# Kernel optimization log

Hardware: AMD Instinct MI355X
Metric: run time of the kernel (lower is better)

The kernel has to match this reference:

```python
import jax, jax.numpy as jnp
import numpy as np

N = 50000   # nodes
E = 600000  # edges
IN = 128    # in_channels
H = 128     # hidden
G = 64      # graphs in batch


def setup_inputs() -> dict:
    key = jax.random.key(0)
    ks = jax.random.split(key, 12)
    x = jax.random.normal(ks[0], (N, IN), jnp.float32)
    edge_index = jax.random.randint(ks[1], (2, E), 0, N, dtype=jnp.int64)
    batch = jnp.sort(jax.random.randint(ks[2], (N,), 0, G, dtype=jnp.int64))

    def glorot(k, i, o):
        return jax.random.normal(k, (i, o), jnp.float32) / np.float32(np.sqrt(i))

    return {
        "x": x, "edge_index": edge_index, "batch": batch,
        "W1": glorot(ks[3], IN, H), "b1": jnp.zeros((H,), jnp.float32),
        "W2": glorot(ks[4], H, H),  "b2": jnp.zeros((H,), jnp.float32),
        "W3": glorot(ks[5], H, H),  "b3": jnp.zeros((H,), jnp.float32),
        "Wl": glorot(ks[6], H, 2),  "bl": jnp.zeros((2,), jnp.float32),
    }


def gcn_conv(x, W, b, src, dst, n):
    # PyG GCNConv: linear transform, add self-loops, symmetric deg^-1/2 norm, scatter-add.
    h = x @ W                                   # [n, H]
    loop = jnp.arange(n, dtype=src.dtype)
    s = jnp.concatenate([src, loop])            # [E+n]
    d = jnp.concatenate([dst, loop])
    deg = jax.ops.segment_sum(jnp.ones_like(d, jnp.float32), d, num_segments=n)
    dinv = jax.lax.rsqrt(deg)                   # deg >= 1 thanks to self-loops
    norm = dinv[s] * dinv[d]                    # [E+n]
    out = jax.ops.segment_sum(h[s] * norm[:, None], d, num_segments=n)
    return out + b


def reference(x, edge_index, batch, W1, b1, W2, b2, W3, b3, Wl, bl):
    src, dst = edge_index[0], edge_index[1]
    h = jax.nn.relu(gcn_conv(x, W1, b1, src, dst, N))
    h = jax.nn.relu(gcn_conv(h, W2, b2, src, dst, N))
    h = jax.nn.relu(gcn_conv(h, W3, b3, src, dst, N))
    # global_mean_pool over graph ids
    cnt = jax.ops.segment_sum(jnp.ones((N,), jnp.float32), batch, num_segments=G)
    pooled = jax.ops.segment_sum(h, batch, num_segments=G) / jnp.maximum(cnt, 1.0)[:, None]
    # dropout is identity in eval mode
    return pooled @ Wl + bl                     # [G, 2]
```

## Files before the change

### kernel.cpp

```cpp
#include <hip/hip_runtime.h>


#define THREADS 256
#define ELLW 48
#define ELLS 64

typedef __attribute__((ext_vector_type(8))) short short8;
typedef __attribute__((ext_vector_type(4))) float f32x4;

__device__ inline unsigned short bf16_1(float a) {
    unsigned u = __float_as_uint(a);
    u += 0x7FFF + ((u >> 16) & 1);
    return (unsigned short)(u >> 16);
}
__device__ inline void bf16_split(float f, unsigned short& hi, unsigned short& lo) {
    unsigned u = __float_as_uint(f);
    unsigned r = u + 0x7FFF + ((u >> 16) & 1);
    hi = (unsigned short)(r >> 16);
    float hf = __uint_as_float((unsigned)hi << 16);
    float lf = f - hf;
    unsigned ul = __float_as_uint(lf);
    lo = (unsigned short)((ul + 0x7FFF + ((ul >> 16) & 1)) >> 16);
}
__device__ inline unsigned pack_bf16(float a, float b) {
    unsigned ua = __float_as_uint(a);
    unsigned ub = __float_as_uint(b);
    ua += 0x7FFF + ((ua >> 16) & 1);
    ub += 0x7FFF + ((ub >> 16) & 1);
    return (ua >> 16) | (ub & 0xFFFF0000u);
}

__global__ __launch_bounds__(THREADS) void prep_k(const float* __restrict__ W1,
                                                  const float* __restrict__ W2,
                                                  const float* __restrict__ W3,
                                                  unsigned* __restrict__ wf,
                                                  const int* __restrict__ batch,
                                                  int* __restrict__ gstart,
                                                  int* __restrict__ ell,
                                                  int n, int gtot) {
    int b = blockIdx.x;
    if (b < 3) {
        const float* W = (b == 0) ? W1 : (b == 1) ? W2 : W3;
        unsigned* o_hi = wf + (size_t)b * 16384;
        unsigned* o_lo = o_hi + 8192;
        for (int o = threadIdx.x; o < 8192; o += THREADS) {
            int d = o & 3, l = (o >> 2) & 63, ts = o >> 8;
            int s = ts & 3, t = ts >> 2;
            int k = s * 32 + ((l >> 4) << 3) + d * 2;
            int nn = t * 16 + (l & 15);
            float v0 = W[k * 128 + nn];
            float v1 = W[(k + 1) * 128 + nn];
            unsigned short h0, l0, h1, l1;
            bf16_split(v0, h0, l0);
            bf16_split(v1, h1, l1);
            o_hi[o] = (unsigned)h0 | ((unsigned)h1 << 16);
            o_lo[o] = (unsigned)l0 | ((unsigned)l1 << 16);
        }
    } else if (b == 3) {
        int t = threadIdx.x;
        if (t <= gtot) {
            int lo = 0, hi = n;
            while (lo < hi) {
                int mid = (lo + hi) >> 1;
                if (batch[mid] < t) lo = mid + 1; else hi = mid;
            }
            gstart[t] = lo;
        }
    } else {
        int i = (b - 4) * THREADS + threadIdx.x;
        if (i < n) ell[(size_t)i * ELLS] = 0;
    }
}

__global__ __launch_bounds__(THREADS) void ell_fill_k(const int* __restrict__ src,
                                                      const int* __restrict__ dst,
                                                      int* __restrict__ ell, int e) {
    int i = blockIdx.x * THREADS + threadIdx.x;
    if (i < e) {
        int d = dst[i];
        int* row = ell + (size_t)d * ELLS;
        int pos = atomicAdd(row, 1);
        if (pos < ELLW) row[1 + pos] = src[i];
    }
}

template <bool ABF16>
__global__ __launch_bounds__(THREADS) void mfma_gemm_k(const void* __restrict__ Av,
                                                       const unsigned* __restrict__ wf,
                                                       const int* __restrict__ ell,
                                                       unsigned short* __restrict__ g16u,
                                                       int n) {
    __shared__ unsigned wls[16384];
    int tid = threadIdx.x;
    int lane = tid & 63;
    int r0 = blockIdx.x * 64 + (tid >> 6) * 16;

    for (int i = tid; i < 4096; i += THREADS)
        ((uint4*)wls)[i] = ((const uint4*)wf)[i];

    f32x4 acc[8];
#pragma unroll
    for (int t = 0; t < 8; ++t) acc[t] = (f32x4){0.f, 0.f, 0.f, 0.f};

    int arow = min(r0 + (lane & 15), n - 1);
    int kcol = (lane >> 4) << 3;

    short8 ah[4], al[4];
    if (ABF16) {
        const unsigned short* A = (const unsigned short*)Av;
#pragma unroll
        for (int s = 0; s < 4; ++s)
            ah[s] = *(const short8*)&A[(size_t)arow * 128 + kcol + s * 32];
    } else {
        const float* A = (const float*)Av;
        float4 v0[4], v1[4];
#pragma unroll
        for (int s = 0; s < 4; ++s) {
            v0[s] = *(const float4*)&A[(size_t)arow * 128 + kcol + s * 32];
            v1[s] = *(const float4*)&A[(size_t)arow * 128 + kcol + s * 32 + 4];
        }
#pragma unroll
        for (int s = 0; s < 4; ++s) {
            unsigned short h[8], lo[8];
            bf16_split(v0[s].x, h[0], lo[0]); bf16_split(v0[s].y, h[1], lo[1]);
            bf16_split(v0[s].z, h[2], lo[2]); bf16_split(v0[s].w, h[3], lo[3]);
            bf16_split(v1[s].x, h[4], lo[4]); bf16_split(v1[s].y, h[5], lo[5]);
            bf16_split(v1[s].z, h[6], lo[6]); bf16_split(v1[s].w, h[7], lo[7]);
#pragma unroll
            for (int j = 0; j < 8; ++j) { ah[s][j] = (short)h[j]; al[s][j] = (short)lo[j]; }
        }
    }

    __syncthreads();

#pragma unroll
    for (int s = 0; s < 4; ++s) {
#pragma unroll
        for (int t = 0; t < 8; ++t) {
            int base = (t * 4 + s) * 256 + lane * 4;
            short8 bh = *(short8*)&wls[base];
            short8 bl = *(short8*)&wls[8192 + base];
            acc[t] = __builtin_amdgcn_mfma_f32_16x16x32_bf16(ah[s], bh, acc[t], 0, 0, 0);
            if (!ABF16)
                acc[t] = __builtin_amdgcn_mfma_f32_16x16x32_bf16(al[s], bh, acc[t], 0, 0, 0);
            acc[t] = __builtin_amdgcn_mfma_f32_16x16x32_bf16(ah[s], bl, acc[t], 0, 0, 0);
        }
    }

    int rbase = r0 + ((lane >> 4) << 2);
#pragma unroll
    for (int reg = 0; reg < 4; ++reg) {
        int rr = rbase + reg;
        if (rr < n) {
            float dv = rsqrtf(1.f + (float)ell[(size_t)rr * ELLS]);
#pragma unroll
            for (int t = 0; t < 8; ++t)
                g16u[(size_t)rr * 128 + t * 16 + (lane & 15)] = bf16_1(acc[t][reg] * dv);
        }
    }
}

__global__ __launch_bounds__(THREADS) void aggregate_k(const unsigned* __restrict__ g16,
                                                       const int* __restrict__ ell,
                                                       const float* __restrict__ bias,
                                                       unsigned* __restrict__ h16,
                                                       int n) {
    int wave = (blockIdx.x * THREADS + threadIdx.x) >> 6;
    int lane = threadIdx.x & 63;
    if (wave >= n) return;

    int v = ell[(size_t)wave * ELLS + lane];
    int cnt_true = __shfl(v, 0);
    int deg = min(cnt_true, ELLW);

    unsigned us = g16[(size_t)wave * 64 + lane];
    float ax0 = __uint_as_float(us << 16);
    float ay0 = __uint_as_float(us & 0xFFFF0000u);
    float ax1 = 0.f, ay1 = 0.f, ax2 = 0.f, ay2 = 0.f, ax3 = 0.f, ay3 = 0.f;
    float ax4 = 0.f, ay4 = 0.f, ax5 = 0.f, ay5 = 0.f, ax6 = 0.f, ay6 = 0.f;
    float ax7 = 0.f, ay7 = 0.f;

    for (int k = 0; k < deg; k += 8) {
        int s0 = __shfl(v, k + 1);
        int s1 = __shfl(v, min(k + 2, deg));
        int s2 = __shfl(v, min(k + 3, deg));
        int s3 = __shfl(v, min(k + 4, deg));
        int s4 = __shfl(v, min(k + 5, deg));
        int s5 = __shfl(v, min(k + 6, deg));
        int s6 = __shfl(v, min(k + 7, deg));
        int s7 = __shfl(v, min(k + 8, deg));
        float m1 = (k + 1 < deg) ? 1.f : 0.f;
        float m2 = (k + 2 < deg) ? 1.f : 0.f;
        float m3 = (k + 3 < deg) ? 1.f : 0.f;
        float m4 = (k + 4 < deg) ? 1.f : 0.f;
        float m5 = (k + 5 < deg) ? 1.f : 0.f;
        float m6 = (k + 6 < deg) ? 1.f : 0.f;
        float m7 = (k + 7 < deg) ? 1.f : 0.f;
        unsigned u0 = g16[(size_t)s0 * 64 + lane];
        unsigned u1 = g16[(size_t)s1 * 64 + lane];
        unsigned u2 = g16[(size_t)s2 * 64 + lane];
        unsigned u3 = g16[(size_t)s3 * 64 + lane];
        unsigned u4 = g16[(size_t)s4 * 64 + lane];
        unsigned u5 = g16[(size_t)s5 * 64 + lane];
        unsigned u6 = g16[(size_t)s6 * 64 + lane];
        unsigned u7 = g16[(size_t)s7 * 64 + lane];
        ax0 += __uint_as_float(u0 << 16);
        ay0 += __uint_as_float(u0 & 0xFFFF0000u);
        ax1 = fmaf(m1, __uint_as_float(u1 << 16), ax1);
        ay1 = fmaf(m1, __uint_as_float(u1 & 0xFFFF0000u), ay1);
        ax2 = fmaf(m2, __uint_as_float(u2 << 16), ax2);
        ay2 = fmaf(m2, __uint_as_float(u2 & 0xFFFF0000u), ay2);
        ax3 = fmaf(m3, __uint_as_float(u3 << 16), ax3);
        ay3 = fmaf(m3, __uint_as_float(u3 & 0xFFFF0000u), ay3);
        ax4 = fmaf(m4, __uint_as_float(u4 << 16), ax4);
        ay4 = fmaf(m4, __uint_as_float(u4 & 0xFFFF0000u), ay4);
        ax5 = fmaf(m5, __uint_as_float(u5 << 16), ax5);
        ay5 = fmaf(m5, __uint_as_float(u5 & 0xFFFF0000u), ay5);
        ax6 = fmaf(m6, __uint_as_float(u6 << 16), ax6);
        ay6 = fmaf(m6, __uint_as_float(u6 & 0xFFFF0000u), ay6);
        ax7 = fmaf(m7, __uint_as_float(u7 << 16), ax7);
        ay7 = fmaf(m7, __uint_as_float(u7 & 0xFFFF0000u), ay7);
    }
    ax0 += (ax1 + ax2) + (ax3 + ax4) + (ax5 + ax6) + ax7;
    ay0 += (ay1 + ay2) + (ay3 + ay4) + (ay5 + ay6) + ay7;

    float d = rsqrtf(1.f + (float)cnt_true);
    float2 bb = ((const float2*)bias)[lane];
    float ox = fmaxf(fmaf(d, ax0, bb.x), 0.f);
    float oy = fmaxf(fmaf(d, ay0, bb.y), 0.f);
    h16[(size_t)wave * 64 + lane] = pack_bf16(ox, oy);
}

#define PSLICES 8
__global__ __launch_bounds__(THREADS) void pool_k(const unsigned* __restrict__ h16,
                                                  const int* __restrict__ gstart,
                                                  float* __restrict__ partial) {
    int gph = blockIdx.x, s = blockIdx.y;
    int start = gstart[gph], end = gstart[gph + 1];
    int len = end - start;
    int chunk = (len + PSLICES - 1) / PSLICES;
    int rs = start + s * chunk;
    int re = min(rs + chunk, end);
    int c = threadIdx.x & 63, half = threadIdx.x >> 6;
    float sx = 0.f, sy = 0.f;
    for (int r = rs + half; r < re; r += 4) {
        unsigned u = h16[(size_t)r * 64 + c];
        sx += __uint_as_float(u << 16);
        sy += __uint_as_float(u & 0xFFFF0000u);
    }
    __shared__ float shx[4][64], shy[4][64];
    shx[half][c] = sx;
    shy[half][c] = sy;
    __syncthreads();
    if (half == 0) {
        sx = shx[0][c] + shx[1][c] + shx[2][c] + shx[3][c];
        sy = shy[0][c] + shy[1][c] + shy[2][c] + shy[3][c];
        partial[(gph * PSLICES + s) * 128 + c * 2] = sx;
        partial[(gph * PSLICES + s) * 128 + c * 2 + 1] = sy;
    }
}

__global__ __launch_bounds__(128) void final_k(const float* __restrict__ partial,
                                               const int* __restrict__ gstart,
                                               const float* __restrict__ Wl,
                                               const float* __restrict__ bl,
                                               float* __restrict__ out, int gtot) {
    int t = threadIdx.x;
    int gph = t >> 1, j = t & 1;
    if (gph >= gtot) return;
    float cnt = fmaxf((float)(gstart[gph + 1] - gstart[gph]), 1.f);
    float sacc = 0.f;
    for (int k = 0; k < 128; ++k) {
        float v = 0.f;
#pragma unroll
        for (int sb = 0; sb < PSLICES; ++sb)
            v += partial[(gph * PSLICES + sb) * 128 + k];
        sacc = fmaf(v, Wl[k * 2 + j], sacc);
    }
    out[gph * 2 + j] = sacc / cnt + bl[j];
}

extern "C" void kernel_launch(void* const* d_in, const int* in_sizes, int n_in,
                              void* d_out, int out_size, void* d_ws, size_t ws_size,
                              hipStream_t stream) {
    const float* x  = (const float*)d_in[0];
    const int* ei   = (const int*)d_in[1];
    const int* batch= (const int*)d_in[2];
    const float* W1 = (const float*)d_in[3];
    const float* b1 = (const float*)d_in[4];
    const float* W2 = (const float*)d_in[5];
    const float* b2 = (const float*)d_in[6];
    const float* W3 = (const float*)d_in[7];
    const float* b3 = (const float*)d_in[8];
    const float* Wl = (const float*)d_in[9];
    const float* bl = (const float*)d_in[10];
    float* out = (float*)d_out;

    const int N = in_sizes[0] / 128;
    const int E = in_sizes[1] / 2;
    const int G = out_size / 2;
    const int* src = ei;
    const int* dst = ei + E;

    char* ws = (char*)d_ws;
    size_t off = 0;
    auto alloc = [&](size_t bytes) -> void* {
        void* p = ws + off;
        off = (off + bytes + 255) & ~(size_t)255;
        return p;
    };
    unsigned* g16  = (unsigned*)alloc((size_t)N * 64 * 4);
    unsigned* h16  = (unsigned*)alloc((size_t)N * 64 * 4);
    int* ell       = (int*)alloc((size_t)N * ELLS * 4);
    unsigned* wf   = (unsigned*)alloc((size_t)3 * 16384 * 4);
    float* partial = (float*)alloc((size_t)G * PSLICES * 128 * 4);
    int* gstart    = (int*)alloc((size_t)(G + 1) * 4);
    (void)ws_size;

    int gridE = (E + THREADS - 1) / THREADS;
    int gridN = (N + THREADS - 1) / THREADS;

    prep_k<<<4 + gridN, THREADS, 0, stream>>>(W1, W2, W3, wf, batch, gstart, ell, N, G);
    ell_fill_k<<<gridE, THREADS, 0, stream>>>(src, dst, ell, E);

    int gemmGrid = (N + 63) / 64;
    int aggGrid = (N + 3) / 4;
    unsigned short* g16u = (unsigned short*)g16;

    mfma_gemm_k<false><<<gemmGrid, THREADS, 0, stream>>>(x, wf, ell, g16u, N);
    aggregate_k<<<aggGrid, THREADS, 0, stream>>>(g16, ell, b1, h16, N);
    mfma_gemm_k<true><<<gemmGrid, THREADS, 0, stream>>>(h16, wf + 16384, ell, g16u, N);
    aggregate_k<<<aggGrid, THREADS, 0, stream>>>(g16, ell, b2, h16, N);
    mfma_gemm_k<true><<<gemmGrid, THREADS, 0, stream>>>(h16, wf + 32768, ell, g16u, N);
    aggregate_k<<<aggGrid, THREADS, 0, stream>>>(g16, ell, b3, h16, N);

    dim3 poolGrid(G, PSLICES);
    pool_k<<<poolGrid, THREADS, 0, stream>>>(h16, gstart, partial);
    final_k<<<1, 128, 0, stream>>>(partial, gstart, Wl, bl, out, G);
}
```

Before: 193.9 us.

## Pack ELL neighbor indices as 16-bit and aggregate two nodes per wave

Neighbor indices in the ELL table are now stored as 16-bit values, which halves the row stride to 32 ints, and the edge fill writes ushorts. The aggregation kernel handles two destination nodes per wave: each half-wave loads one node's row and the loop issues 16 gathers per iteration for more memory-level parallelism. N is 50000, so indices fit in 16 bits, but this silently caps supported graph size at 65536 nodes. The paired loop runs to the larger of the two degrees, so the lower-degree node does masked redundant loads.

```diff
diff --git a/kernel.cpp b/kernel.cpp
--- a/kernel.cpp
+++ b/kernel.cpp
@@ -3,7 +3,7 @@
 
 #define THREADS 256
 #define ELLW 48
-#define ELLS 64
+#define ELLD 32
 
 typedef __attribute__((ext_vector_type(8))) short short8;
 typedef __attribute__((ext_vector_type(4))) float f32x4;
@@ -68,7 +68,7 @@
         }
     } else {
         int i = (b - 4) * THREADS + threadIdx.x;
-        if (i < n) ell[(size_t)i * ELLS] = 0;
+        if (i < n) ell[(size_t)i * ELLD] = 0;
     }
 }
 
@@ -78,9 +78,9 @@
     int i = blockIdx.x * THREADS + threadIdx.x;
     if (i < e) {
         int d = dst[i];
-        int* row = ell + (size_t)d * ELLS;
+        int* row = ell + (size_t)d * ELLD;
         int pos = atomicAdd(row, 1);
-        if (pos < ELLW) row[1 + pos] = src[i];
+        if (pos < ELLW) ((unsigned short*)row)[2 + pos] = (unsigned short)src[i];
     }
 }
 
@@ -152,7 +152,7 @@
     for (int reg = 0; reg < 4; ++reg) {
         int rr = rbase + reg;
         if (rr < n) {
-            float dv = rsqrtf(1.f + (float)ell[(size_t)rr * ELLS]);
+            float dv = rsqrtf(1.f + (float)ell[(size_t)rr * ELLD]);
 #pragma unroll
             for (int t = 0; t < 8; ++t)
                 g16u[(size_t)rr * 128 + t * 16 + (lane & 15)] = bf16_1(acc[t][reg] * dv);
@@ -161,74 +161,75 @@
 }
 
 __global__ __launch_bounds__(THREADS) void aggregate_k(const unsigned* __restrict__ g16,
-                                                       const int* __restrict__ ell,
+                                                       const unsigned* __restrict__ ell,
                                                        const float* __restrict__ bias,
                                                        unsigned* __restrict__ h16,
                                                        int n) {
-    int wave = (blockIdx.x * THREADS + threadIdx.x) >> 6;
+    int w = (blockIdx.x * THREADS + threadIdx.x) >> 6;
     int lane = threadIdx.x & 63;
-    if (wave >= n) return;
-
-    int v = ell[(size_t)wave * ELLS + lane];
-    int cnt_true = __shfl(v, 0);
-    int deg = min(cnt_true, ELLW);
-
-    unsigned us = g16[(size_t)wave * 64 + lane];
-    float ax0 = __uint_as_float(us << 16);
-    float ay0 = __uint_as_float(us & 0xFFFF0000u);
-    float ax1 = 0.f, ay1 = 0.f, ax2 = 0.f, ay2 = 0.f, ax3 = 0.f, ay3 = 0.f;
-    float ax4 = 0.f, ay4 = 0.f, ax5 = 0.f, ay5 = 0.f, ax6 = 0.f, ay6 = 0.f;
-    float ax7 = 0.f, ay7 = 0.f;
-
-    for (int k = 0; k < deg; k += 8) {
-        int s0 = __shfl(v, k + 1);
-        int s1 = __shfl(v, min(k + 2, deg));
-        int s2 = __shfl(v, min(k + 3, deg));
-        int s3 = __shfl(v, min(k + 4, deg));
-        int s4 = __shfl(v, min(k + 5, deg));
-        int s5 = __shfl(v, min(k + 6, deg));
-        int s6 = __shfl(v, min(k + 7, deg));
-        int s7 = __shfl(v, min(k + 8, deg));
-        float m1 = (k + 1 < deg) ? 1.f : 0.f;
-        float m2 = (k + 2 < deg) ? 1.f : 0.f;
-        float m3 = (k + 3 < deg) ? 1.f : 0.f;
-        float m4 = (k + 4 < deg) ? 1.f : 0.f;
-        float m5 = (k + 5 < deg) ? 1.f : 0.f;
-        float m6 = (k + 6 < deg) ? 1.f : 0.f;
-        float m7 = (k + 7 < deg) ? 1.f : 0.f;
-        unsigned u0 = g16[(size_t)s0 * 64 + lane];
-        unsigned u1 = g16[(size_t)s1 * 64 + lane];
-        unsigned u2 = g16[(size_t)s2 * 64 + lane];
-        unsigned u3 = g16[(size_t)s3 * 64 + lane];
-        unsigned u4 = g16[(size_t)s4 * 64 + lane];
-        unsigned u5 = g16[(size_t)s5 * 64 + lane];
-        unsigned u6 = g16[(size_t)s6 * 64 + lane];
-        unsigned u7 = g16[(size_t)s7 * 64 + lane];
-        ax0 += __uint_as_float(u0 << 16);
-        ay0 += __uint_as_float(u0 & 0xFFFF0000u);
-        ax1 = fmaf(m1, __uint_as_float(u1 << 16), ax1);
-        ay1 = fmaf(m1, __uint_as_float(u1 & 0xFFFF0000u), ay1);
-        ax2 = fmaf(m2, __uint_as_float(u2 << 16), ax2);
-        ay2 = fmaf(m2, __uint_as_float(u2 & 0xFFFF0000u), ay2);
-        ax3 = fmaf(m3, __uint_as_float(u3 << 16), ax3);
-        ay3 = fmaf(m3, __uint_as_float(u3 & 0xFFFF0000u), ay3);
-        ax4 = fmaf(m4, __uint_as_float(u4 << 16), ax4);
-        ay4 = fmaf(m4, __uint_as_float(u4 & 0xFFFF0000u), ay4);
-        ax5 = fmaf(m5, __uint_as_float(u5 << 16), ax5);
-        ay5 = fmaf(m5, __uint_as_float(u5 & 0xFFFF0000u), ay5);
-        ax6 = fmaf(m6, __uint_as_float(u6 << 16), ax6);
-        ay6 = fmaf(m6, __uint_as_float(u6 & 0xFFFF0000u), ay6);
-        ax7 = fmaf(m7, __uint_as_float(u7 << 16), ax7);
-        ay7 = fmaf(m7, __uint_as_float(u7 & 0xFFFF0000u), ay7);
-    }
-    ax0 += (ax1 + ax2) + (ax3 + ax4) + (ax5 + ax6) + ax7;
-    ay0 += (ay1 + ay2) + (ay3 + ay4) + (ay5 + ay6) + ay7;
-
-    float d = rsqrtf(1.f + (float)cnt_true);
+    int n0 = w * 2;
+    if (n0 >= n) return;
+    int has1 = (n0 + 1 < n);
+    int nsel = lane >> 5;
+    int nidx = min(n0 + nsel, n - 1);
+    unsigned v = ell[(size_t)nidx * ELLD + (lane & 31)];
+    int cnt0 = (int)__shfl(v, 0);
+    int cnt1 = has1 ? (int)__shfl(v, 32) : 0;
+    int deg0 = min(cnt0, ELLW), deg1 = min(cnt1, ELLW);
+    int c0 = max(deg0 - 1, 0), c1 = max(deg1 - 1, 0);
+    int nm1 = n - 1;
+
+    unsigned us0 = g16[(size_t)n0 * 64 + lane];
+    unsigned us1 = g16[(size_t)min(n0 + 1, nm1) * 64 + lane];
+    float A0x = __uint_as_float(us0 << 16), A0y = __uint_as_float(us0 & 0xFFFF0000u);
+    float B0x = 0.f, B0y = 0.f;
+    float A1x = __uint_as_float(us1 << 16), A1y = __uint_as_float(us1 & 0xFFFF0000u);
+    float B1x = 0.f, B1y = 0.f;
+
+    int maxd = max(deg0, deg1);
+    for (int k = 0; k < maxd; k += 8) {
+        int s0[8], s1[8];
+        float m0[8], m1[8];
+#pragma unroll
+        for (int j = 0; j < 8; ++j) {
+            int jj0 = min(k + j, c0);
+            unsigned d0 = __shfl(v, 1 + (jj0 >> 1));
+            s0[j] = min((int)((d0 >> ((jj0 & 1) * 16)) & 0xFFFFu), nm1);
+            m0[j] = (k + j < deg0) ? 1.f : 0.f;
+            int jj1 = min(k + j, c1);
+            unsigned d1 = __shfl(v, 33 + (jj1 >> 1));
+            s1[j] = min((int)((d1 >> ((jj1 & 1) * 16)) & 0xFFFFu), nm1);
+            m1[j] = (k + j < deg1) ? 1.f : 0.f;
+        }
+        unsigned u0[8], u1[8];
+#pragma unroll
+        for (int j = 0; j < 8; ++j) u0[j] = g16[(size_t)s0[j] * 64 + lane];
+#pragma unroll
+        for (int j = 0; j < 8; ++j) u1[j] = g16[(size_t)s1[j] * 64 + lane];
+#pragma unroll
+        for (int j = 0; j < 8; j += 2) {
+            A0x = fmaf(m0[j], __uint_as_float(u0[j] << 16), A0x);
+            A0y = fmaf(m0[j], __uint_as_float(u0[j] & 0xFFFF0000u), A0y);
+            B0x = fmaf(m0[j + 1], __uint_as_float(u0[j + 1] << 16), B0x);
+            B0y = fmaf(m0[j + 1], __uint_as_float(u0[j + 1] & 0xFFFF0000u), B0y);
+            A1x = fmaf(m1[j], __uint_as_float(u1[j] << 16), A1x);
+            A1y = fmaf(m1[j], __uint_as_float(u1[j] & 0xFFFF0000u), A1y);
+            B1x = fmaf(m1[j + 1], __uint_as_float(u1[j + 1] << 16), B1x);
+            B1y = fmaf(m1[j + 1], __uint_as_float(u1[j + 1] & 0xFFFF0000u), B1y);
+        }
+    }
+
     float2 bb = ((const float2*)bias)[lane];
-    float ox = fmaxf(fmaf(d, ax0, bb.x), 0.f);
-    float oy = fmaxf(fmaf(d, ay0, bb.y), 0.f);
-    h16[(size_t)wave * 64 + lane] = pack_bf16(ox, oy);
+    float d0 = rsqrtf(1.f + (float)cnt0);
+    float ox = fmaxf(fmaf(d0, A0x + B0x, bb.x), 0.f);
+    float oy = fmaxf(fmaf(d0, A0y + B0y, bb.y), 0.f);
+    h16[(size_t)n0 * 64 + lane] = pack_bf16(ox, oy);
+    if (has1) {
+        float d1 = rsqrtf(1.f + (float)cnt1);
+        float px = fmaxf(fmaf(d1, A1x + B1x, bb.x), 0.f);
+        float py = fmaxf(fmaf(d1, A1y + B1y, bb.y), 0.f);
+        h16[(size_t)(n0 + 1) * 64 + lane] = pack_bf16(px, py);
+    }
 }
 
 #define PSLICES 8
@@ -311,7 +312,7 @@
     };
     unsigned* g16  = (unsigned*)alloc((size_t)N * 64 * 4);
     unsigned* h16  = (unsigned*)alloc((size_t)N * 64 * 4);
-    int* ell       = (int*)alloc((size_t)N * ELLS * 4);
+    int* ell       = (int*)alloc((size_t)N * ELLD * 4);
     unsigned* wf   = (unsigned*)alloc((size_t)3 * 16384 * 4);
     float* partial = (float*)alloc((size_t)G * PSLICES * 128 * 4);
     int* gstart    = (int*)alloc((size_t)(G + 1) * 4);
@@ -324,15 +325,15 @@
     ell_fill_k<<<gridE, THREADS, 0, stream>>>(src, dst, ell, E);
 
     int gemmGrid = (N + 63) / 64;
-    int aggGrid = (N + 3) / 4;
+    int aggGrid = (N + 7) / 8;
     unsigned short* g16u = (unsigned short*)g16;
 
     mfma_gemm_k<false><<<gemmGrid, THREADS, 0, stream>>>(x, wf, ell, g16u, N);
-    aggregate_k<<<aggGrid, THREADS, 0, stream>>>(g16, ell, b1, h16, N);
+    aggregate_k<<<aggGrid, THREADS, 0, stream>>>(g16, (const unsigned*)ell, b1, h16, N);
     mfma_gemm_k<true><<<gemmGrid, THREADS, 0, stream>>>(h16, wf + 16384, ell, g16u, N);
-    aggregate_k<<<aggGrid, THREADS, 0, stream>>>(g16, ell, b2, h16, N);
+    aggregate_k<<<aggGrid, THREADS, 0, stream>>>(g16, (const unsigned*)ell, b2, h16, N);
     mfma_gemm_k<true><<<gemmGrid, THREADS, 0, stream>>>(h16, wf + 32768, ell, g16u, N);
-    aggregate_k<<<aggGrid, THREADS, 0, stream>>>(g16, ell, b3, h16, N);
+    aggregate_k<<<aggGrid, THREADS, 0, stream>>>(g16, (const unsigned*)ell, b3, h16, N);
 
     dim3 poolGrid(G, PSLICES);
     pool_k<<<poolGrid, THREADS, 0, stream>>>(h16, gstart, partial);
```

Result: slower. 210.7 us (+8.7%).
